# Kernel tuning notes

Measured on AMD Instinct MI355X. Metric: run time of the kernel, lower is better.

The kernel has to match this reference:

```python
import jax, jax.numpy as jnp
import numpy as np

N, M, D, K = 32768, 8192, 384, 9


def setup_inputs() -> dict:
    key = jax.random.key(0)
    k1, k2 = jax.random.split(key)
    return {
        "embedding": jax.random.normal(k1, (N, D), dtype=jnp.float32),
        "memory_bank": jax.random.normal(k2, (M, D), dtype=jnp.float32),
        "n_neighbors": K,
    }


def reference(embedding, memory_bank, n_neighbors):
    x_norm = jnp.sum(embedding * embedding, axis=-1, keepdims=True)      # [N, 1]
    y_norm = jnp.sum(memory_bank * memory_bank, axis=-1, keepdims=True)  # [M, 1]
    d2 = x_norm - 2.0 * jnp.matmul(embedding, memory_bank.T) + y_norm.T  # [N, M]
    dist = jnp.sqrt(jnp.maximum(d2, 0.0))
    # topk smallest along dim 1 (patch_scores, indices discarded)
    neg_top, _ = jax.lax.top_k(-dist, n_neighbors)
    patch_scores = -neg_top  # [N, K], ascending distances
    return patch_scores
```

## Files before the change

kernel.cpp:

```cpp
#include <hip/hip_runtime.h>
#include <hip/hip_bf16.h>

#define N_ROWS 32768
#define M_ROWS 8192
#define D_DIM  384
#define K_NB   9
#define BN     64
#define MQ     (M_ROWS / 4)
#define TILES  (MQ / BN)
#define KP     6

#define QRANGE 2048.0f
#define QSCALE (1.0f / 2048.0f)
#define QSTEPF (QRANGE / 65535.0f)
#define M2S    (-2.0f * QSCALE)
#define BIGF   3.0e38f

#define YS_OFF 49152

typedef long i64;
typedef __attribute__((ext_vector_type(2))) long i64x2;
typedef __attribute__((ext_vector_type(4))) float f32x4;
typedef __attribute__((ext_vector_type(4))) unsigned u32x4;

__global__ __launch_bounds__(256) void FAPM_prep8(
    const float* __restrict__ emb, const float* __restrict__ mem,
    unsigned* __restrict__ A8, unsigned* __restrict__ B8,
    float* __restrict__ xn, float* __restrict__ yn) {
  const int lane = threadIdx.x & 63;
  const int row  = blockIdx.x * 4 + (threadIdx.x >> 6);
  const float* src;
  unsigned* dst;
  float* nptr;
  if (row < N_ROWS) {
    src = emb + (size_t)row * D_DIM; dst = A8 + (size_t)row * 96; nptr = xn + row;
  } else {
    int r = row - N_ROWS;
    src = mem + (size_t)r * D_DIM; dst = B8 + (size_t)r * 96; nptr = yn + r;
  }
  float s = 0.f;
  {
    int dw = lane;
    int kp = dw >> 4, r4 = dw & 15;
    int grp = r4 >> 2, half = (r4 >> 1) & 1, j = (r4 & 1) * 4;
    int k0 = kp * 64 + half * 32 + grp * 8 + j;
    f32x4 v = *(const f32x4*)(src + k0);
    s += v.x * v.x + v.y * v.y + v.z * v.z + v.w * v.w;
    int pk = __builtin_amdgcn_cvt_pk_fp8_f32(v.x, v.y, 0, false);
    pk = __builtin_amdgcn_cvt_pk_fp8_f32(v.z, v.w, pk, true);
    dst[dw] = (unsigned)pk;
  }
  if (lane < 32) {
    int dw = lane + 64;
    int kp = dw >> 4, r4 = dw & 15;
    int grp = r4 >> 2, half = (r4 >> 1) & 1, j = (r4 & 1) * 4;
    int k0 = kp * 64 + half * 32 + grp * 8 + j;
    f32x4 v = *(const f32x4*)(src + k0);
    s += v.x * v.x + v.y * v.y + v.z * v.z + v.w * v.w;
    int pk = __builtin_amdgcn_cvt_pk_fp8_f32(v.x, v.y, 0, false);
    pk = __builtin_amdgcn_cvt_pk_fp8_f32(v.z, v.w, pk, true);
    dst[dw] = (unsigned)pk;
  }
#pragma unroll
  for (int dd = 1; dd < 64; dd <<= 1) s += __shfl_xor(s, dd);
  if (lane == 0) *nptr = s;
}

__device__ __forceinline__ unsigned pkmin(unsigned a, unsigned b) {
  unsigned d;
  asm("v_pk_min_u16 %0, %1, %2" : "=v"(d) : "v"(a), "v"(b));
  return d;
}
__device__ __forceinline__ unsigned pkmax(unsigned a, unsigned b) {
  unsigned d;
  asm("v_pk_max_u16 %0, %1, %2" : "=v"(d) : "v"(a), "v"(b));
  return d;
}

__device__ __forceinline__ void merge16i(unsigned t[9], float* dst, int sub) {
  for (int s = 0; s < K_NB; ++s) {
    unsigned m  = t[0];
    int      ml = sub;
#pragma unroll
    for (int dd = 1; dd < 16; dd <<= 1) {
      unsigned ov = (unsigned)__shfl_xor((int)m, dd);
      int      ol = __shfl_xor(ml, dd);
      bool take = (ov < m) || (ov == m && ol < ml);
      m  = take ? ov : m;
      ml = take ? ol : ml;
    }
    if (sub == ml) {
#pragma unroll
      for (int j = 0; j < 8; ++j) t[j] = t[j + 1];
      t[8] = 0xFFFFu;
    }
    if (sub == 0) dst[s] = (float)m * QSTEPF;
  }
}

__global__ __launch_bounds__(256, 3) void FAPM_fused(
    const unsigned char* __restrict__ A8, const unsigned char* __restrict__ B8,
    const float* __restrict__ xn, const float* __restrict__ yn,
    float* __restrict__ part) {
  __shared__ __attribute__((aligned(128))) unsigned char LDS[53248];
  const int tid  = threadIdx.x;
  const int lane = tid & 63;
  const int w    = tid >> 6;
  const int sub  = lane & 15;
  const int grp  = lane >> 4;
  const int bx   = blockIdx.x;
  const int mq   = bx & 3;
  const int wrow0 = (bx >> 2) * 128 + w * 32;
  const int colbase = mq * MQ;

  float xs0[4], xs1[4];
#pragma unroll
  for (int i = 0; i < 4; ++i) {
    xs0[i] = xn[wrow0 + grp * 4 + i] * QSCALE;
    xs1[i] = xn[wrow0 + 16 + grp * 4 + i] * QSCALE;
  }

  {
    const float* yp = yn + colbase + tid * 8;
    f32x4 v0 = *(const f32x4*)yp;
    f32x4 v1 = *(const f32x4*)(yp + 4);
    float a0 = v0.x * QSCALE, a1 = v0.y * QSCALE, a2 = v0.z * QSCALE, a3 = v0.w * QSCALE;
    float a4 = v1.x * QSCALE, a5 = v1.y * QSCALE, a6 = v1.z * QSCALE, a7 = v1.w * QSCALE;
    unsigned q0, q1, q2, q3;
    asm("v_cvt_pknorm_u16_f32 %0, %1, %2" : "=v"(q0) : "v"(a0), "v"(a1));
    asm("v_cvt_pknorm_u16_f32 %0, %1, %2" : "=v"(q1) : "v"(a2), "v"(a3));
    asm("v_cvt_pknorm_u16_f32 %0, %1, %2" : "=v"(q2) : "v"(a4), "v"(a5));
    asm("v_cvt_pknorm_u16_f32 %0, %1, %2" : "=v"(q3) : "v"(a6), "v"(a7));
    *(u32x4*)(&LDS[YS_OFF + tid * 16]) = (u32x4){q0, q1, q2, q3};
  }

  {
    const unsigned char* asrc = A8 + (size_t)(wrow0 + sub) * D_DIM + grp * 16;
#pragma unroll
    for (int rb = 0; rb < 2; ++rb)
#pragma unroll
      for (int q = 0; q < KP; ++q)
        __builtin_amdgcn_global_load_lds(
            (const __attribute__((address_space(1))) void*)(asrc + rb * 16 * D_DIM + q * 64),
            (__attribute__((address_space(3))) void*)(LDS + ((w * 2 + rb) * KP + q) * 1024),
            16, 0, 0);
  }
  asm volatile("s_waitcnt vmcnt(0)" ::: "memory");
  __syncthreads();

  i64 af0[12], af1[12];
  {
    const unsigned char* ar0 = LDS + (w * 2) * (KP * 1024) + lane * 16;
    const unsigned char* ar1 = ar0 + KP * 1024;
#pragma unroll
    for (int kp = 0; kp < KP; ++kp) {
      i64x2 v0 = *(const i64x2*)(ar0 + kp * 1024);
      i64x2 v1 = *(const i64x2*)(ar1 + kp * 1024);
      af0[2 * kp] = v0.x; af0[2 * kp + 1] = v0.y;
      af1[2 * kp] = v1.x; af1[2 * kp + 1] = v1.y;
    }
  }
  __syncthreads();

  const unsigned char* bsrc = B8 + (size_t)(colbase + w * 16 + sub) * D_DIM + grp * 16;
#pragma unroll
  for (int q = 0; q < KP; ++q)
    __builtin_amdgcn_global_load_lds(
        (const __attribute__((address_space(1))) void*)(bsrc + q * 64),
        (__attribute__((address_space(3))) void*)(LDS + (w * KP + q) * 1024),
        16, 0, 0);
#pragma unroll
  for (int q = 0; q < KP; ++q)
    __builtin_amdgcn_global_load_lds(
        (const __attribute__((address_space(1))) void*)(bsrc + 24576 + q * 64),
        (__attribute__((address_space(3))) void*)(LDS + 24576 + (w * KP + q) * 1024),
        16, 0, 0);
  bsrc += 2 * 24576;

  unsigned tkp[4][9];
#pragma unroll
  for (int i = 0; i < 4; ++i)
#pragma unroll
    for (int j = 0; j < 9; ++j) tkp[i][j] = 0xFFFFFFFFu;

  for (int t = 0; t < TILES; ++t) {
    const int bufo = (t & 1) * 24576;
    if (t + 1 < TILES) asm volatile("s_waitcnt vmcnt(6)" ::: "memory");
    else               asm volatile("s_waitcnt vmcnt(0)" ::: "memory");
    __builtin_amdgcn_s_barrier();

    const unsigned char* br = LDS + bufo + lane * 16;
#pragma unroll
    for (int cb = 0; cb < 4; ++cb) {
      unsigned yu = *(const unsigned short*)(
          &LDS[YS_OFF + ((t * 64 + cb * 16 + sub) << 1)]);
      float ysv = (float)yu * (1.0f / 65535.0f);

      f32x4 acc0 = {0.f, 0.f, 0.f, 0.f}, acc1 = {0.f, 0.f, 0.f, 0.f};
      __builtin_amdgcn_s_setprio(1);
#pragma unroll
      for (int kp = 0; kp < KP; ++kp) {
        i64x2 b = *(const i64x2*)(br + (cb * KP + kp) * 1024);
        acc0 = __builtin_amdgcn_mfma_f32_16x16x32_fp8_fp8(af0[2 * kp], b.x, acc0, 0, 0, 0);
        acc1 = __builtin_amdgcn_mfma_f32_16x16x32_fp8_fp8(af1[2 * kp], b.x, acc1, 0, 0, 0);
        acc0 = __builtin_amdgcn_mfma_f32_16x16x32_fp8_fp8(af0[2 * kp + 1], b.y, acc0, 0, 0, 0);
        acc1 = __builtin_amdgcn_mfma_f32_16x16x32_fp8_fp8(af1[2 * kp + 1], b.y, acc1, 0, 0, 0);
      }
      __builtin_amdgcn_s_setprio(0);

#pragma unroll
      for (int i = 0; i < 4; ++i) {
        float d2a = fmaf(acc0[i], M2S, xs0[i] + ysv);
        float d2b = fmaf(acc1[i], M2S, xs1[i] + ysv);
        unsigned dp;
        asm("v_cvt_pknorm_u16_f32 %0, %1, %2" : "=v"(dp) : "v"(d2a), "v"(d2b));
#pragma unroll
        for (int j = 8; j >= 1; --j)
          tkp[i][j] = pkmin(tkp[i][j], pkmax(dp, tkp[i][j - 1]));
        tkp[i][0] = pkmin(tkp[i][0], dp);
      }
    }
    __builtin_amdgcn_s_barrier();

    if (t + 2 < TILES) {
#pragma unroll
      for (int q = 0; q < KP; ++q)
        __builtin_amdgcn_global_load_lds(
            (const __attribute__((address_space(1))) void*)(bsrc + q * 64),
            (__attribute__((address_space(3))) void*)(LDS + bufo + (w * KP + q) * 1024),
            16, 0, 0);
      bsrc += 24576;
    }
  }

  float* pbase = part + (size_t)mq * N_ROWS * K_NB;
#pragma unroll
  for (int i = 0; i < 4; ++i) {
    unsigned ta[9], tb[9];
#pragma unroll
    for (int j = 0; j < 9; ++j) { ta[j] = tkp[i][j] & 0xFFFFu; tb[j] = tkp[i][j] >> 16; }
    merge16i(ta, pbase + (size_t)(wrow0 + grp * 4 + i) * K_NB, sub);
    merge16i(tb, pbase + (size_t)(wrow0 + 16 + grp * 4 + i) * K_NB, sub);
  }
}

__global__ __launch_bounds__(256) void FAPM_merge4(
    const float* __restrict__ part, float* __restrict__ out) {
  const int r = blockIdx.x * 256 + threadIdx.x;
  float l[4][9];
#pragma unroll
  for (int q = 0; q < 4; ++q)
#pragma unroll
    for (int j = 0; j < 9; ++j)
      l[q][j] = part[(size_t)q * N_ROWS * K_NB + (size_t)r * K_NB + j];
#pragma unroll
  for (int s = 0; s < K_NB; ++s) {
    float m = fminf(fminf(l[0][0], l[1][0]), fminf(l[2][0], l[3][0]));
    out[(size_t)r * K_NB + s] = sqrtf(fmaxf(m, 0.f));
    bool t0 = (l[0][0] == m);
    bool t1 = (l[1][0] == m) && !t0;
    bool t2 = (l[2][0] == m) && !t0 && !t1;
    bool t3 = !(t0 || t1 || t2);
#pragma unroll
    for (int j = 0; j < 8; ++j) {
      l[0][j] = t0 ? l[0][j + 1] : l[0][j];
      l[1][j] = t1 ? l[1][j + 1] : l[1][j];
      l[2][j] = t2 ? l[2][j + 1] : l[2][j];
      l[3][j] = t3 ? l[3][j + 1] : l[3][j];
    }
    l[0][8] = t0 ? BIGF : l[0][8];
    l[1][8] = t1 ? BIGF : l[1][8];
    l[2][8] = t2 ? BIGF : l[2][8];
    l[3][8] = t3 ? BIGF : l[3][8];
  }
}

extern "C" void kernel_launch(void* const* d_in, const int* in_sizes, int n_in,
                              void* d_out, int out_size, void* d_ws, size_t ws_size,
                              hipStream_t stream) {
  const float* emb = (const float*)d_in[0];
  const float* mem = (const float*)d_in[1];
  float* out = (float*)d_out;
  char* ws = (char*)d_ws;
  size_t offA = 0;
  size_t offB = offA + (size_t)N_ROWS * D_DIM;
  size_t offX = offB + (size_t)M_ROWS * D_DIM;
  size_t offY = offX + (size_t)N_ROWS * 4;
  size_t offP = offY + (size_t)M_ROWS * 4;
  unsigned char* A8 = (unsigned char*)(ws + offA);
  unsigned char* B8 = (unsigned char*)(ws + offB);
  float* xn = (float*)(ws + offX);
  float* yn = (float*)(ws + offY);
  float* part = (float*)(ws + offP);

  FAPM_prep8<<<(N_ROWS + M_ROWS) / 4, 256, 0, stream>>>(
      emb, mem, (unsigned*)A8, (unsigned*)B8, xn, yn);
  FAPM_fused<<<(N_ROWS / 128) * 4, 256, 0, stream>>>(A8, B8, xn, yn, part);
  FAPM_merge4<<<N_ROWS / 256, 256, 0, stream>>>(part, out);
}
```

Measured before the change: 225.0 us.

## Switch to 16x16x128 scaled FP8 MFMA, 256-row blocks, defer x-norm to merge

Replaces the 16x16x32 fp8 MFMA with the gfx950 16x16x128 scaled f8f6f4 MFMA, which needs a plain row-major fp8 layout in prep. Each block now covers 256 embedding rows, so each wave holds 64 rows of A in registers and reuses every B fragment across four MFMAs. The per-row x-norm is removed from the hot loop and added back in the merge kernel, with a y offset and a matching offset correction keeping the u16-quantized distances non-negative. The larger register footprint lowers occupancy to 2 blocks per SIMD set and changes the quantization range.

```diff
diff --git a/kernel.cpp b/kernel.cpp
--- a/kernel.cpp
+++ b/kernel.cpp
@@ -6,22 +6,29 @@
 #define D_DIM  384
 #define K_NB   9
 #define BN     64
+#define BM     256
 #define MQ     (M_ROWS / 4)
 #define TILES  (MQ / BN)
-#define KP     6
-
-#define QRANGE 2048.0f
+#define KS     3
+
 #define QSCALE (1.0f / 2048.0f)
-#define QSTEPF (QRANGE / 65535.0f)
-#define M2S    (-2.0f * QSCALE)
+#define YOFF   0.125f
+#define QSTEPF (2048.0f / 65535.0f)
+#define QOFFB  256.0f
+#define M2S    (-2.0f / 2048.0f)
 #define BIGF   3.0e38f
 
 #define YS_OFF 49152
 
-typedef long i64;
-typedef __attribute__((ext_vector_type(2))) long i64x2;
-typedef __attribute__((ext_vector_type(4))) float f32x4;
+typedef __attribute__((ext_vector_type(4))) int      i32x4;
+typedef __attribute__((ext_vector_type(8))) int      i32x8;
+typedef __attribute__((ext_vector_type(4))) float    f32x4;
 typedef __attribute__((ext_vector_type(4))) unsigned u32x4;
+
+#define GLDS(SRC, DST)                                                       \
+  __builtin_amdgcn_global_load_lds(                                          \
+      (const __attribute__((address_space(1))) void*)(SRC),                  \
+      (__attribute__((address_space(3))) void*)(DST), 16, 0, 0)
 
 __global__ __launch_bounds__(256) void FAPM_prep8(
     const float* __restrict__ emb, const float* __restrict__ mem,
@@ -41,10 +48,7 @@
   float s = 0.f;
   {
     int dw = lane;
-    int kp = dw >> 4, r4 = dw & 15;
-    int grp = r4 >> 2, half = (r4 >> 1) & 1, j = (r4 & 1) * 4;
-    int k0 = kp * 64 + half * 32 + grp * 8 + j;
-    f32x4 v = *(const f32x4*)(src + k0);
+    f32x4 v = *(const f32x4*)(src + dw * 4);
     s += v.x * v.x + v.y * v.y + v.z * v.z + v.w * v.w;
     int pk = __builtin_amdgcn_cvt_pk_fp8_f32(v.x, v.y, 0, false);
     pk = __builtin_amdgcn_cvt_pk_fp8_f32(v.z, v.w, pk, true);
@@ -52,10 +56,7 @@
   }
   if (lane < 32) {
     int dw = lane + 64;
-    int kp = dw >> 4, r4 = dw & 15;
-    int grp = r4 >> 2, half = (r4 >> 1) & 1, j = (r4 & 1) * 4;
-    int k0 = kp * 64 + half * 32 + grp * 8 + j;
-    f32x4 v = *(const f32x4*)(src + k0);
+    f32x4 v = *(const f32x4*)(src + dw * 4);
     s += v.x * v.x + v.y * v.y + v.z * v.z + v.w * v.w;
     int pk = __builtin_amdgcn_cvt_pk_fp8_f32(v.x, v.y, 0, false);
     pk = __builtin_amdgcn_cvt_pk_fp8_f32(v.z, v.w, pk, true);
@@ -94,14 +95,13 @@
       for (int j = 0; j < 8; ++j) t[j] = t[j + 1];
       t[8] = 0xFFFFu;
     }
-    if (sub == 0) dst[s] = (float)m * QSTEPF;
-  }
-}
-
-__global__ __launch_bounds__(256, 3) void FAPM_fused(
+    if (sub == 0) dst[s] = (float)m * QSTEPF - QOFFB;
+  }
+}
+
+__global__ __launch_bounds__(256, 2) void FAPM_fused(
     const unsigned char* __restrict__ A8, const unsigned char* __restrict__ B8,
-    const float* __restrict__ xn, const float* __restrict__ yn,
-    float* __restrict__ part) {
+    const float* __restrict__ yn, float* __restrict__ part) {
   __shared__ __attribute__((aligned(128))) unsigned char LDS[53248];
   const int tid  = threadIdx.x;
   const int lane = tid & 63;
@@ -110,22 +110,17 @@
   const int grp  = lane >> 4;
   const int bx   = blockIdx.x;
   const int mq   = bx & 3;
-  const int wrow0 = (bx >> 2) * 128 + w * 32;
+  const int row0 = (bx >> 2) * BM;
   const int colbase = mq * MQ;
-
-  float xs0[4], xs1[4];
-#pragma unroll
-  for (int i = 0; i < 4; ++i) {
-    xs0[i] = xn[wrow0 + grp * 4 + i] * QSCALE;
-    xs1[i] = xn[wrow0 + 16 + grp * 4 + i] * QSCALE;
-  }
 
   {
     const float* yp = yn + colbase + tid * 8;
     f32x4 v0 = *(const f32x4*)yp;
     f32x4 v1 = *(const f32x4*)(yp + 4);
-    float a0 = v0.x * QSCALE, a1 = v0.y * QSCALE, a2 = v0.z * QSCALE, a3 = v0.w * QSCALE;
-    float a4 = v1.x * QSCALE, a5 = v1.y * QSCALE, a6 = v1.z * QSCALE, a7 = v1.w * QSCALE;
+    float a0 = fmaf(v0.x, QSCALE, YOFF), a1 = fmaf(v0.y, QSCALE, YOFF);
+    float a2 = fmaf(v0.z, QSCALE, YOFF), a3 = fmaf(v0.w, QSCALE, YOFF);
+    float a4 = fmaf(v1.x, QSCALE, YOFF), a5 = fmaf(v1.y, QSCALE, YOFF);
+    float a6 = fmaf(v1.z, QSCALE, YOFF), a7 = fmaf(v1.w, QSCALE, YOFF);
     unsigned q0, q1, q2, q3;
     asm("v_cvt_pknorm_u16_f32 %0, %1, %2" : "=v"(q0) : "v"(a0), "v"(a1));
     asm("v_cvt_pknorm_u16_f32 %0, %1, %2" : "=v"(q1) : "v"(a2), "v"(a3));
@@ -134,54 +129,60 @@
     *(u32x4*)(&LDS[YS_OFF + tid * 16]) = (u32x4){q0, q1, q2, q3};
   }
 
-  {
-    const unsigned char* asrc = A8 + (size_t)(wrow0 + sub) * D_DIM + grp * 16;
-#pragma unroll
-    for (int rb = 0; rb < 2; ++rb)
-#pragma unroll
-      for (int q = 0; q < KP; ++q)
-        __builtin_amdgcn_global_load_lds(
-            (const __attribute__((address_space(1))) void*)(asrc + rb * 16 * D_DIM + q * 64),
-            (__attribute__((address_space(3))) void*)(LDS + ((w * 2 + rb) * KP + q) * 1024),
-            16, 0, 0);
-  }
-  asm volatile("s_waitcnt vmcnt(0)" ::: "memory");
-  __syncthreads();
-
-  i64 af0[12], af1[12];
-  {
-    const unsigned char* ar0 = LDS + (w * 2) * (KP * 1024) + lane * 16;
-    const unsigned char* ar1 = ar0 + KP * 1024;
-#pragma unroll
-    for (int kp = 0; kp < KP; ++kp) {
-      i64x2 v0 = *(const i64x2*)(ar0 + kp * 1024);
-      i64x2 v1 = *(const i64x2*)(ar1 + kp * 1024);
-      af0[2 * kp] = v0.x; af0[2 * kp + 1] = v0.y;
-      af1[2 * kp] = v1.x; af1[2 * kp + 1] = v1.y;
-    }
-  }
-  __syncthreads();
-
-  const unsigned char* bsrc = B8 + (size_t)(colbase + w * 16 + sub) * D_DIM + grp * 16;
-#pragma unroll
-  for (int q = 0; q < KP; ++q)
-    __builtin_amdgcn_global_load_lds(
-        (const __attribute__((address_space(1))) void*)(bsrc + q * 64),
-        (__attribute__((address_space(3))) void*)(LDS + (w * KP + q) * 1024),
-        16, 0, 0);
-#pragma unroll
-  for (int q = 0; q < KP; ++q)
-    __builtin_amdgcn_global_load_lds(
-        (const __attribute__((address_space(1))) void*)(bsrc + 24576 + q * 64),
-        (__attribute__((address_space(3))) void*)(LDS + 24576 + (w * KP + q) * 1024),
-        16, 0, 0);
+  i32x8 af[4][KS];
+
+#pragma unroll
+  for (int half = 0; half < 2; ++half) {
+    const unsigned char* asrc =
+        A8 + (size_t)(row0 + half * 128 + (w * 2) * 16 + (lane & 15)) * D_DIM +
+        (lane >> 4) * 32;
+#pragma unroll
+    for (int rb2 = 0; rb2 < 2; ++rb2)
+#pragma unroll
+      for (int ks = 0; ks < KS; ++ks)
+#pragma unroll
+        for (int h = 0; h < 2; ++h)
+          GLDS(asrc + rb2 * 16 * D_DIM + ks * 128 + h * 16,
+               LDS + (((w * 2 + rb2) * KS + ks) * 2 + h) * 1024);
+    asm volatile("s_waitcnt vmcnt(0)" ::: "memory");
+    __syncthreads();
+    if ((w >> 1) == half) {
+      const int rbh = (w & 1) * 4;
+#pragma unroll
+      for (int rbl = 0; rbl < 4; ++rbl)
+#pragma unroll
+        for (int ks = 0; ks < KS; ++ks) {
+          const unsigned char* p =
+              LDS + (((rbh + rbl) * KS + ks) * 2) * 1024 + lane * 16;
+          *(i32x4*)&af[rbl][ks] = *(const i32x4*)p;
+          *((i32x4*)&af[rbl][ks] + 1) = *(const i32x4*)(p + 1024);
+        }
+    }
+    __syncthreads();
+  }
+
+  const unsigned char* bsrc =
+      B8 + (size_t)(colbase + w * 16 + (lane & 15)) * D_DIM + (lane >> 4) * 32;
+#pragma unroll
+  for (int ks = 0; ks < KS; ++ks)
+#pragma unroll
+    for (int h = 0; h < 2; ++h)
+      GLDS(bsrc + ks * 128 + h * 16, LDS + w * 6144 + (ks * 2 + h) * 1024);
+#pragma unroll
+  for (int ks = 0; ks < KS; ++ks)
+#pragma unroll
+    for (int h = 0; h < 2; ++h)
+      GLDS(bsrc + 24576 + ks * 128 + h * 16,
+           LDS + 24576 + w * 6144 + (ks * 2 + h) * 1024);
   bsrc += 2 * 24576;
 
-  unsigned tkp[4][9];
-#pragma unroll
-  for (int i = 0; i < 4; ++i)
-#pragma unroll
-    for (int j = 0; j < 9; ++j) tkp[i][j] = 0xFFFFFFFFu;
+  unsigned tkp[2][4][9];
+#pragma unroll
+  for (int s2 = 0; s2 < 2; ++s2)
+#pragma unroll
+    for (int i = 0; i < 4; ++i)
+#pragma unroll
+      for (int j = 0; j < 9; ++j) tkp[s2][i][j] = 0xFFFFFFFFu;
 
   for (int t = 0; t < TILES; ++t) {
     const int bufo = (t & 1) * 24576;
@@ -196,57 +197,75 @@
           &LDS[YS_OFF + ((t * 64 + cb * 16 + sub) << 1)]);
       float ysv = (float)yu * (1.0f / 65535.0f);
 
-      f32x4 acc0 = {0.f, 0.f, 0.f, 0.f}, acc1 = {0.f, 0.f, 0.f, 0.f};
+      i32x8 bf[KS];
+#pragma unroll
+      for (int ks = 0; ks < KS; ++ks) {
+        const unsigned char* p = br + cb * 6144 + ks * 2048;
+        *(i32x4*)&bf[ks] = *(const i32x4*)p;
+        *((i32x4*)&bf[ks] + 1) = *(const i32x4*)(p + 1024);
+      }
+      f32x4 acc[4];
+#pragma unroll
+      for (int rbl = 0; rbl < 4; ++rbl) acc[rbl] = (f32x4){0.f, 0.f, 0.f, 0.f};
       __builtin_amdgcn_s_setprio(1);
 #pragma unroll
-      for (int kp = 0; kp < KP; ++kp) {
-        i64x2 b = *(const i64x2*)(br + (cb * KP + kp) * 1024);
-        acc0 = __builtin_amdgcn_mfma_f32_16x16x32_fp8_fp8(af0[2 * kp], b.x, acc0, 0, 0, 0);
-        acc1 = __builtin_amdgcn_mfma_f32_16x16x32_fp8_fp8(af1[2 * kp], b.x, acc1, 0, 0, 0);
-        acc0 = __builtin_amdgcn_mfma_f32_16x16x32_fp8_fp8(af0[2 * kp + 1], b.y, acc0, 0, 0, 0);
-        acc1 = __builtin_amdgcn_mfma_f32_16x16x32_fp8_fp8(af1[2 * kp + 1], b.y, acc1, 0, 0, 0);
+      for (int ks = 0; ks < KS; ++ks)
+#pragma unroll
+        for (int rbl = 0; rbl < 4; ++rbl)
+          acc[rbl] = __builtin_amdgcn_mfma_scale_f32_16x16x128_f8f6f4(
+              af[rbl][ks], bf[ks], acc[rbl], 0, 0,
+              0, 0x7F7F7F7F, 0, 0x7F7F7F7F);
+      __builtin_amdgcn_s_setprio(0);
+
+#pragma unroll
+      for (int s2 = 0; s2 < 2; ++s2)
+#pragma unroll
+        for (int i = 0; i < 4; ++i) {
+          float d2a = fmaf(acc[2 * s2][i], M2S, ysv);
+          float d2b = fmaf(acc[2 * s2 + 1][i], M2S, ysv);
+          unsigned dp;
+          asm("v_cvt_pknorm_u16_f32 %0, %1, %2" : "=v"(dp) : "v"(d2a), "v"(d2b));
+#pragma unroll
+          for (int j = 8; j >= 1; --j)
+            tkp[s2][i][j] = pkmin(tkp[s2][i][j], pkmax(dp, tkp[s2][i][j - 1]));
+          tkp[s2][i][0] = pkmin(tkp[s2][i][0], dp);
+        }
+    }
+    __builtin_amdgcn_s_barrier();
+
+    if (t + 2 < TILES) {
+#pragma unroll
+      for (int ks = 0; ks < KS; ++ks)
+#pragma unroll
+        for (int h = 0; h < 2; ++h)
+          GLDS(bsrc + ks * 128 + h * 16,
+               LDS + bufo + w * 6144 + (ks * 2 + h) * 1024);
+      bsrc += 24576;
+    }
+  }
+
+  float* pbase = part + (size_t)mq * N_ROWS * K_NB;
+#pragma unroll
+  for (int s2 = 0; s2 < 2; ++s2)
+#pragma unroll
+    for (int i = 0; i < 4; ++i) {
+      unsigned ta[9], tb[9];
+#pragma unroll
+      for (int j = 0; j < 9; ++j) {
+        ta[j] = tkp[s2][i][j] & 0xFFFFu;
+        tb[j] = tkp[s2][i][j] >> 16;
       }
-      __builtin_amdgcn_s_setprio(0);
-
-#pragma unroll
-      for (int i = 0; i < 4; ++i) {
-        float d2a = fmaf(acc0[i], M2S, xs0[i] + ysv);
-        float d2b = fmaf(acc1[i], M2S, xs1[i] + ysv);
-        unsigned dp;
-        asm("v_cvt_pknorm_u16_f32 %0, %1, %2" : "=v"(dp) : "v"(d2a), "v"(d2b));
-#pragma unroll
-        for (int j = 8; j >= 1; --j)
-          tkp[i][j] = pkmin(tkp[i][j], pkmax(dp, tkp[i][j - 1]));
-        tkp[i][0] = pkmin(tkp[i][0], dp);
-      }
-    }
-    __builtin_amdgcn_s_barrier();
-
-    if (t + 2 < TILES) {
-#pragma unroll
-      for (int q = 0; q < KP; ++q)
-        __builtin_amdgcn_global_load_lds(
-            (const __attribute__((address_space(1))) void*)(bsrc + q * 64),
-            (__attribute__((address_space(3))) void*)(LDS + bufo + (w * KP + q) * 1024),
-            16, 0, 0);
-      bsrc += 24576;
-    }
-  }
-
-  float* pbase = part + (size_t)mq * N_ROWS * K_NB;
-#pragma unroll
-  for (int i = 0; i < 4; ++i) {
-    unsigned ta[9], tb[9];
-#pragma unroll
-    for (int j = 0; j < 9; ++j) { ta[j] = tkp[i][j] & 0xFFFFu; tb[j] = tkp[i][j] >> 16; }
-    merge16i(ta, pbase + (size_t)(wrow0 + grp * 4 + i) * K_NB, sub);
-    merge16i(tb, pbase + (size_t)(wrow0 + 16 + grp * 4 + i) * K_NB, sub);
-  }
+      int rowA = row0 + w * 64 + (2 * s2) * 16 + grp * 4 + i;
+      merge16i(ta, pbase + (size_t)rowA * K_NB, sub);
+      merge16i(tb, pbase + (size_t)(rowA + 16) * K_NB, sub);
+    }
 }
 
 __global__ __launch_bounds__(256) void FAPM_merge4(
-    const float* __restrict__ part, float* __restrict__ out) {
+    const float* __restrict__ part, const float* __restrict__ xn,
+    float* __restrict__ out) {
   const int r = blockIdx.x * 256 + threadIdx.x;
+  const float xr = xn[r];
   float l[4][9];
 #pragma unroll
   for (int q = 0; q < 4; ++q)
@@ -256,7 +275,7 @@
 #pragma unroll
   for (int s = 0; s < K_NB; ++s) {
     float m = fminf(fminf(l[0][0], l[1][0]), fminf(l[2][0], l[3][0]));
-    out[(size_t)r * K_NB + s] = sqrtf(fmaxf(m, 0.f));
+    out[(size_t)r * K_NB + s] = sqrtf(fmaxf(m + xr, 0.f));
     bool t0 = (l[0][0] == m);
     bool t1 = (l[1][0] == m) && !t0;
     bool t2 = (l[2][0] == m) && !t0 && !t1;
@@ -295,6 +314,6 @@
 
   FAPM_prep8<<<(N_ROWS + M_ROWS) / 4, 256, 0, stream>>>(
       emb, mem, (unsigned*)A8, (unsigned*)B8, xn, yn);
-  FAPM_fused<<<(N_ROWS / 128) * 4, 256, 0, stream>>>(A8, B8, xn, yn, part);
-  FAPM_merge4<<<N_ROWS / 256, 256, 0, stream>>>(part, out);
-}
+  FAPM_fused<<<(N_ROWS / BM) * 4, 256, 0, stream>>>(A8, B8, yn, part);
+  FAPM_merge4<<<N_ROWS / 256, 256, 0, stream>>>(part, xn, out);
+}
```

Result: faster. 192.5 us (-14.5%).
